# Kernel optimization log

Hardware: AMD Instinct MI355X
Metric: run time of the kernel (lower is better)

The kernel has to match this reference:

```python
import jax, jax.numpy as jnp
from jax import lax
import numpy as np

NEG_SLOPE = 0.01  # torch leaky_relu default
KSIZE = 5

def lrelu(x):
    return jax.nn.leaky_relu(x, NEG_SLOPE)

def conv(x, w, b):
    # x: [N,C,H,W], w: [O,I,kh,kw], valid padding (pad=False in ConvChain)
    y = lax.conv_general_dilated(x, w, (1, 1), 'VALID',
                                 dimension_numbers=('NCHW', 'OIHW', 'NCHW'))
    return y + b[None, :, None, None]

def _forward(features, radiance, global_features,
             emb_w0, emb_b0, emb_w, emb_b,
             pf_w0, pf_b0, pf_w1, pf_b1, pf_w2, pf_b2,
             sf_w, sf_b,
             kp_w0, kp_b0, kp_w1, kp_b1, kp_w2, kp_b2):
    bs, spp, nf, h, w = features.shape
    ngf = global_features.shape[1]
    K = KSIZE

    # --- sample_embedding over all samples at once (replaces per-sp loop) ---
    g = jnp.broadcast_to(global_features, (bs, ngf, h, w))
    x = jnp.concatenate(
        [jnp.broadcast_to(g[:, None], (bs, spp, ngf, h, w)), features], axis=2)
    x = x.reshape(bs * spp, ngf + nf, h, w)
    x = lrelu(conv(x, emb_w0, emb_b0))
    for i in range(5):  # hidden conv layers 1..5
        x = lrelu(conv(x, emb_w[i], emb_b[i]))
    x = conv(x, emb_w[5], emb_b[5])  # linear output layer
    pixel_embed = x.reshape(bs, spp, x.shape[1], x.shape[2], x.shape[3]).max(axis=1)

    # --- pixel_features chain (3 layers, last linear) ---
    p = lrelu(conv(pixel_embed, pf_w0, pf_b0))
    p = lrelu(conv(p, pf_w1, pf_b1))
    pfeat = conv(p, pf_w2, pf_b2)  # [bs, pair_width, ph, pw]
    ph, pw = pfeat.shape[2], pfeat.shape[3]

    # --- crop features/radiance so needed = ph + K - 1 ---
    needed = ph + K - 1
    crop = (h - needed) // 2
    feat_c = features[..., crop:crop + needed, crop:crop + needed]
    rad_c = radiance[..., crop:crop + needed, crop:crop + needed]

    # --- gather K*K taps per pixel (unfold) ---
    taps = jnp.stack([feat_c[..., dy:dy + ph, dx:dx + pw]
                      for dy in range(K) for dx in range(K)], axis=0)
    # [K,K,bs,spp,nf,ph,pw] -> [bs,ph,pw,spp,ky,kx,nf]
    taps = taps.reshape(K, K, bs, spp, nf, ph, pw).transpose(2, 5, 6, 3, 0, 1, 4)
    off = jnp.arange(K, dtype=taps.dtype) - K // 2
    taps = taps.at[..., 0].add(off)            # x += kx - K//2 (kx axis)
    taps = taps.at[..., 1].add(off[:, None])   # y += ky - K//2 (ky axis)

    rt = jnp.stack([rad_c[..., dy:dy + ph, dx:dx + pw]
                    for dy in range(K) for dx in range(K)], axis=0)
    # [K,K,bs,spp,3,ph,pw] -> [bs,3,ph,pw,spp,ky,kx]
    rt = rt.reshape(K, K, bs, spp, 3, ph, pw).transpose(2, 4, 5, 6, 3, 0, 1)

    # --- sample_features: single linear layer (FullyConnected depth=1) ---
    sf = jnp.einsum('...f,of->...o', taps, sf_w) + sf_b  # [b,ph,pw,spp,ky,kx,pair]

    # --- kernel_predictor on pixel_features + sample_features ---
    pairf = pfeat.transpose(0, 2, 3, 1)[:, :, :, None, None, None, :]
    hdd = lrelu(jnp.einsum('...i,oi->...o', pairf + sf, kp_w0) + kp_b0)
    hdd = lrelu(jnp.einsum('...i,oi->...o', hdd, kp_w1) + kp_b1)
    wts = (jnp.einsum('...i,oi->...o', hdd, kp_w2) + kp_b2)[..., 0]  # [b,ph,pw,spp,ky,kx]

    # --- weighted radiance accumulate + normalize ---
    unnorm = jnp.einsum('bhwsyx,bchwsyx->bchw', wts, rt)
    sumw = wts.sum(axis=(3, 4, 5))[:, None]  # [b,1,ph,pw]
    return unnorm / (sumw + 1e-8)


def setup_inputs() -> dict:
    key = jax.random.key(0)
    ks = jax.random.split(key, 24)
    BS, SPP, NF, NGF, H, W = 1, 4, 12, 4, 116, 116
    WIDTH, PAIR = 128, 64
    s = 0.05
    inp = {}
    inp['features'] = jax.random.normal(ks[0], (BS, SPP, NF, H, W), jnp.float32)
    inp['radiance'] = jax.random.uniform(ks[1], (BS, SPP, 3, H, W), jnp.float32)
    inp['global_features'] = jax.random.normal(ks[2], (BS, NGF, 1, 1), jnp.float32)
    # sample_embedding: 7 conv layers (first 16->128, rest 128->128, last linear)
    inp['emb_w0'] = jax.random.normal(ks[3], (WIDTH, NF + NGF, 3, 3)) * s
    inp['emb_b0'] = jax.random.normal(ks[4], (WIDTH,)) * s
    inp['emb_w'] = jax.random.normal(ks[5], (6, WIDTH, WIDTH, 3, 3)) * s
    inp['emb_b'] = jax.random.normal(ks[6], (6, WIDTH)) * s
    # pixel_features: 3 conv layers 128->128->128->64 (last linear)
    inp['pf_w0'] = jax.random.normal(ks[7], (WIDTH, WIDTH, 3, 3)) * s
    inp['pf_b0'] = jax.random.normal(ks[8], (WIDTH,)) * s
    inp['pf_w1'] = jax.random.normal(ks[9], (WIDTH, WIDTH, 3, 3)) * s
    inp['pf_b1'] = jax.random.normal(ks[10], (WIDTH,)) * s
    inp['pf_w2'] = jax.random.normal(ks[11], (PAIR, WIDTH, 3, 3)) * s
    inp['pf_b2'] = jax.random.normal(ks[12], (PAIR,)) * s
    # sample_features: FullyConnected(12 -> 64, depth=1) = single linear
    inp['sf_w'] = jax.random.normal(ks[13], (PAIR, NF)) * s
    inp['sf_b'] = jax.random.normal(ks[14], (PAIR,)) * s
    # kernel_predictor: FullyConnected(64 -> 1, depth=3)
    inp['kp_w0'] = jax.random.normal(ks[15], (PAIR, PAIR)) * s
    inp['kp_b0'] = jax.random.normal(ks[16], (PAIR,)) * s
    inp['kp_w1'] = jax.random.normal(ks[17], (PAIR, PAIR)) * s
    inp['kp_b1'] = jax.random.normal(ks[18], (PAIR,)) * s
    inp['kp_w2'] = jax.random.normal(ks[19], (1, PAIR)) * s
    inp['kp_b2'] = jax.random.normal(ks[20], (1,)) * s
    return inp


def reference(features, radiance, global_features,
              emb_w0, emb_b0, emb_w, emb_b,
              pf_w0, pf_b0, pf_w1, pf_b1, pf_w2, pf_b2,
              sf_w, sf_b,
              kp_w0, kp_b0, kp_w1, kp_b1, kp_w2, kp_b2):
    return _forward(features, radiance, global_features,
                    emb_w0, emb_b0, emb_w, emb_b,
                    pf_w0, pf_b0, pf_w1, pf_b1, pf_w2, pf_b2,
                    sf_w, sf_b,
                    kp_w0, kp_b0, kp_w1, kp_b1, kp_w2, kp_b2)
```

## Files before the change

### kernel.cpp

```cpp
#include <hip/hip_runtime.h>


#define HW2 13456
#define NF  12
#define NGF 4

__device__ __forceinline__ float lrelu_f(float x) { return x > 0.f ? x : 0.01f * x; }

__global__ __launch_bounds__(256) void k_buildx0(const float* __restrict__ features,
                                                 const float* __restrict__ gf,
                                                 float* __restrict__ out) {
    int i = blockIdx.x * 256 + threadIdx.x;
    const int total = 4 * 16 * HW2;
    if (i >= total) return;
    int n  = i / (16 * HW2);
    int r  = i - n * (16 * HW2);
    int c  = r / HW2;
    int yx = r - c * HW2;
    float v = (c < NGF) ? gf[c] : features[(n * NF + (c - NGF)) * HW2 + yx];
    out[i] = v;
}

__global__ __launch_bounds__(256) void k_wt(const float* __restrict__ w,
                                            float* __restrict__ wt,
                                            int Cout, int Cin) {
    int i = blockIdx.x * 256 + threadIdx.x;
    int total = Cout * Cin * 9;
    if (i >= total) return;
    int m   = i / (Cin * 9);
    int r   = i - m * (Cin * 9);
    int cin = r / 9;
    int kyx = r - cin * 9;
    wt[(kyx * Cin + cin) * Cout + m] = w[i];
}

__global__ __launch_bounds__(256) void k_wt2(const float* __restrict__ w,
                                             float* __restrict__ wt) {
    int i = blockIdx.x * 256 + threadIdx.x;
    if (i >= 4096) return;
    int o = i >> 6, k = i & 63;
    wt[k * 64 + o] = w[i];
}

template <int CIN, int COUT>
__global__ __launch_bounds__(256) void k_convd(const float* __restrict__ in,
                                               const float* __restrict__ wt,
                                               const float* __restrict__ bias,
                                               float* __restrict__ out,
                                               int H, int W, int relu, int tout) {
    constexpr int MW = COUT / 4;
    const int OH = H - 2, OW = W - 2;
    const int n   = blockIdx.z;
    const int ty0 = blockIdx.y * 8, tx0 = blockIdx.x * 8;

    __shared__ float It[CIN * 100];

    const int tid = threadIdx.x;

    const float* inb = in + (size_t)n * CIN * H * W;
    for (int i = tid; i < CIN * 100; i += 256) {
        int cin = i / 100;
        int r   = i - cin * 100;
        int y   = r / 10;
        int x   = r - y * 10;
        int gy = ty0 + y; if (gy > H - 1) gy = H - 1;
        int gx = tx0 + x; if (gx > W - 1) gx = W - 1;
        It[i] = inb[((size_t)cin * H + gy) * W + gx];
    }
    __syncthreads();

    const int lane  = tid & 63;
    const int wv    = __builtin_amdgcn_readfirstlane(tid >> 6);
    const int ly    = lane >> 3, lx = lane & 7;
    const int lbase = ly * 10 + lx;

    float acc[MW];
    #pragma unroll
    for (int mi = 0; mi < MW; ++mi) acc[mi] = 0.f;

    for (int ky = 0; ky < 3; ++ky) {
        for (int kx = 0; kx < 3; ++kx) {
            const int kyx  = ky * 3 + kx;
            const int aoff = lbase + ky * 10 + kx;
            const float* wrow = wt + (size_t)kyx * CIN * COUT + wv * MW;
            #pragma unroll 8
            for (int cin = 0; cin < CIN; ++cin) {
                float v = It[cin * 100 + aoff];
                const float* wr = wrow + (size_t)cin * COUT;
                #pragma unroll
                for (int mi = 0; mi < MW; ++mi)
                    acc[mi] += wr[mi] * v;
            }
        }
    }

    int oy = ty0 + ly, ox = tx0 + lx;
    if (oy < OH && ox < OW) {
        if (tout) {
            float* ob = out + (size_t)(oy * OW + ox) * COUT;
            #pragma unroll
            for (int mi = 0; mi < MW; ++mi) {
                int m = wv * MW + mi;
                float val = acc[mi] + bias[m];
                if (relu) val = lrelu_f(val);
                ob[m] = val;
            }
        } else {
            #pragma unroll
            for (int mi = 0; mi < MW; ++mi) {
                int m = wv * MW + mi;
                float val = acc[mi] + bias[m];
                if (relu) val = lrelu_f(val);
                out[(((size_t)n * COUT + m) * OH + oy) * OW + ox] = val;
            }
        }
    }
}

__global__ __launch_bounds__(256) void k_sppmax(const float* __restrict__ in,
                                                float* __restrict__ out) {
    int i = blockIdx.x * 256 + threadIdx.x;
    const int total = 128 * 102 * 102;
    if (i >= total) return;
    float m = in[i];
    #pragma unroll
    for (int s = 1; s < 4; ++s) m = fmaxf(m, in[i + s * total]);
    out[i] = m;
}

__global__ __launch_bounds__(256) void k_mlp(const float* __restrict__ features,
                                             const float* __restrict__ pfeat_t,
                                             const float* __restrict__ sf_w,
                                             const float* __restrict__ sf_b,
                                             const float* __restrict__ w0t,
                                             const float* __restrict__ b0,
                                             const float* __restrict__ w1t,
                                             const float* __restrict__ b1,
                                             const float* __restrict__ w2, const float* __restrict__ b2,
                                             float* __restrict__ wts) {
    __shared__ float vx[64][256];
    const int t   = threadIdx.x;
    const int gid = blockIdx.x * 256 + t;
    {
        int p  = gid / 100;
        int r  = gid - p * 100;
        int s  = r / 25;
        int tp = r - s * 25;
        int dy = tp / 5;
        int dx = tp - dy * 5;
        int h  = p / 96;
        int w  = p - h * 96;

        int y = 8 + h + dy, x = 8 + w + dx;
        const float* fb = features + (size_t)(s * NF) * HW2 + (size_t)y * 116 + x;
        float f[12];
        #pragma unroll
        for (int i = 0; i < 12; ++i) f[i] = fb[i * HW2];
        f[0] += (float)(dx - 2);
        f[1] += (float)(dy - 2);

        const float* pft = pfeat_t + (size_t)p * 64;
        #pragma unroll
        for (int o = 0; o < 64; ++o) {
            float a = 0.f;
            #pragma unroll
            for (int i = 0; i < 12; ++i) a += sf_w[o * 12 + i] * f[i];
            a += sf_b[o];
            vx[o][t] = pft[o] + a;
        }
    }
    __syncthreads();

    const int lane = t & 63;
    const int og   = 16 * __builtin_amdgcn_readfirstlane(t >> 6);
    const int tl   = lane * 4;

    {
        float acc[16][4];
        #pragma unroll
        for (int j = 0; j < 16; ++j)
            #pragma unroll
            for (int c = 0; c < 4; ++c) acc[j][c] = 0.f;
        #pragma unroll 4
        for (int k = 0; k < 64; ++k) {
            float4 xv = *(const float4*)(&vx[k][tl]);
            const float* wr = w0t + k * 64 + og;
            #pragma unroll
            for (int j = 0; j < 16; ++j) {
                float wj = wr[j];
                acc[j][0] += wj * xv.x; acc[j][1] += wj * xv.y;
                acc[j][2] += wj * xv.z; acc[j][3] += wj * xv.w;
            }
        }
        __syncthreads();
        #pragma unroll
        for (int j = 0; j < 16; ++j) {
            float bj = b0[og + j];
            float4 ov;
            ov.x = lrelu_f(acc[j][0] + bj); ov.y = lrelu_f(acc[j][1] + bj);
            ov.z = lrelu_f(acc[j][2] + bj); ov.w = lrelu_f(acc[j][3] + bj);
            *(float4*)(&vx[og + j][tl]) = ov;
        }
        __syncthreads();
    }

    {
        float acc[16][4];
        #pragma unroll
        for (int j = 0; j < 16; ++j)
            #pragma unroll
            for (int c = 0; c < 4; ++c) acc[j][c] = 0.f;
        #pragma unroll 4
        for (int k = 0; k < 64; ++k) {
            float4 xv = *(const float4*)(&vx[k][tl]);
            const float* wr = w1t + k * 64 + og;
            #pragma unroll
            for (int j = 0; j < 16; ++j) {
                float wj = wr[j];
                acc[j][0] += wj * xv.x; acc[j][1] += wj * xv.y;
                acc[j][2] += wj * xv.z; acc[j][3] += wj * xv.w;
            }
        }
        __syncthreads();
        #pragma unroll
        for (int j = 0; j < 16; ++j) {
            float bj = b1[og + j];
            float4 ov;
            ov.x = lrelu_f(acc[j][0] + bj); ov.y = lrelu_f(acc[j][1] + bj);
            ov.z = lrelu_f(acc[j][2] + bj); ov.w = lrelu_f(acc[j][3] + bj);
            *(float4*)(&vx[og + j][tl]) = ov;
        }
        __syncthreads();
    }

    {
        float a = 0.f;
        #pragma unroll
        for (int i = 0; i < 64; ++i) a += w2[i] * vx[i][t];
        a += b2[0];
        wts[gid] = a;
    }
}

__global__ __launch_bounds__(256) void k_reduce(const float* __restrict__ wts,
                                                const float* __restrict__ radiance,
                                                float* __restrict__ out) {
    int p = blockIdx.x * 256 + threadIdx.x;
    if (p >= 9216) return;
    int h = p / 96, w = p - h * 96;
    float sw = 0.f, un0 = 0.f, un1 = 0.f, un2 = 0.f;
    const float* wp = wts + (size_t)p * 100;
    for (int s = 0; s < 4; ++s) {
        #pragma unroll
        for (int dy = 0; dy < 5; ++dy) {
            #pragma unroll
            for (int dx = 0; dx < 5; ++dx) {
                float wv = wp[s * 25 + dy * 5 + dx];
                sw += wv;
                int y = 8 + h + dy, x = 8 + w + dx;
                const float* rb = radiance + (size_t)(s * 3) * HW2 + (size_t)y * 116 + x;
                un0 += wv * rb[0 * HW2];
                un1 += wv * rb[1 * HW2];
                un2 += wv * rb[2 * HW2];
            }
        }
    }
    float inv = 1.f / (sw + 1e-8f);
    out[0 * 9216 + p] = un0 * inv;
    out[1 * 9216 + p] = un1 * inv;
    out[2 * 9216 + p] = un2 * inv;
}

extern "C" void kernel_launch(void* const* d_in, const int* in_sizes, int n_in,
                              void* d_out, int out_size, void* d_ws, size_t ws_size,
                              hipStream_t stream) {
    const float* features = (const float*)d_in[0];
    const float* radiance = (const float*)d_in[1];
    const float* gf       = (const float*)d_in[2];
    const float* emb_w0   = (const float*)d_in[3];
    const float* emb_b0   = (const float*)d_in[4];
    const float* emb_w    = (const float*)d_in[5];
    const float* emb_b    = (const float*)d_in[6];
    const float* pf_w0    = (const float*)d_in[7];
    const float* pf_b0    = (const float*)d_in[8];
    const float* pf_w1    = (const float*)d_in[9];
    const float* pf_b1    = (const float*)d_in[10];
    const float* pf_w2    = (const float*)d_in[11];
    const float* pf_b2    = (const float*)d_in[12];
    const float* sf_w     = (const float*)d_in[13];
    const float* sf_b     = (const float*)d_in[14];
    const float* kp_w0    = (const float*)d_in[15];
    const float* kp_b0    = (const float*)d_in[16];
    const float* kp_w1    = (const float*)d_in[17];
    const float* kp_b1    = (const float*)d_in[18];
    const float* kp_w2    = (const float*)d_in[19];
    const float* kp_b2    = (const float*)d_in[20];
    float* out = (float*)d_out;

    float* WT = (float*)d_ws;
    float* wt0  = WT;
    float* wtE0 = WT + 18432;
    float* wtP0 = WT + 18432 + 6 * 147456;
    float* wtP1 = WT + 1050624;
    float* wtP2 = WT + 1198080;
    float* w0t  = WT + 1271808;
    float* w1t  = WT + 1275904;
    float* A = WT + 1280000;
    float* B = A + 6653952;

    auto wtr = [&](const float* w, float* dst, int Cout, int Cin) {
        int total = Cout * Cin * 9;
        k_wt<<<dim3((total + 255) / 256), 256, 0, stream>>>(w, dst, Cout, Cin);
    };
    wtr(emb_w0, wt0, 128, 16);
    for (int i = 0; i < 6; ++i) wtr(emb_w + i * 147456, wtE0 + i * 147456, 128, 128);
    wtr(pf_w0, wtP0, 128, 128);
    wtr(pf_w1, wtP1, 128, 128);
    wtr(pf_w2, wtP2, 64, 128);
    k_wt2<<<dim3(16), 256, 0, stream>>>(kp_w0, w0t);
    k_wt2<<<dim3(16), 256, 0, stream>>>(kp_w1, w1t);

    k_buildx0<<<dim3((4 * 16 * HW2 + 255) / 256), 256, 0, stream>>>(features, gf, A);

    auto grid8 = [](int OH, int OW, int N) {
        return dim3((OW + 7) / 8, (OH + 7) / 8, N);
    };

    k_convd<16, 128><<<grid8(114, 114, 4), 256, 0, stream>>>(A, wt0, emb_b0, B, 116, 116, 1, 0);
    k_convd<128,128><<<grid8(112, 112, 4), 256, 0, stream>>>(B, wtE0 + 0*147456, emb_b + 0*128, A, 114, 114, 1, 0);
    k_convd<128,128><<<grid8(110, 110, 4), 256, 0, stream>>>(A, wtE0 + 1*147456, emb_b + 1*128, B, 112, 112, 1, 0);
    k_convd<128,128><<<grid8(108, 108, 4), 256, 0, stream>>>(B, wtE0 + 2*147456, emb_b + 2*128, A, 110, 110, 1, 0);
    k_convd<128,128><<<grid8(106, 106, 4), 256, 0, stream>>>(A, wtE0 + 3*147456, emb_b + 3*128, B, 108, 108, 1, 0);
    k_convd<128,128><<<grid8(104, 104, 4), 256, 0, stream>>>(B, wtE0 + 4*147456, emb_b + 4*128, A, 106, 106, 1, 0);
    k_convd<128,128><<<grid8(102, 102, 4), 256, 0, stream>>>(A, wtE0 + 5*147456, emb_b + 5*128, B, 104, 104, 0, 0);

    k_sppmax<<<dim3(1331712 / 256), 256, 0, stream>>>(B, A);

    k_convd<128,128><<<grid8(100, 100, 1), 256, 0, stream>>>(A, wtP0, pf_b0, B, 102, 102, 1, 0);
    k_convd<128,128><<<grid8(98,  98,  1), 256, 0, stream>>>(B, wtP1, pf_b1, A, 100, 100, 1, 0);
    k_convd<128, 64><<<grid8(96,  96,  1), 256, 0, stream>>>(A, wtP2, pf_b2, B, 98,  98,  0, 1);

    k_mlp<<<dim3(3600), 256, 0, stream>>>(features, B, sf_w, sf_b,
                                          w0t, kp_b0, w1t, kp_b1, kp_w2, kp_b2, A);

    k_reduce<<<dim3(36), 256, 0, stream>>>(A, radiance, out);
}
```

Before: 2.643 ms.

## Replace LDS-tiled conv with direct-load kernel splitting output channels across blocks

The 3x3 conv kernel no longer stages an input tile in shared memory. Each thread now reads its input taps straight from global memory and computes two output rows across 16 output channels per wave, and output channels are split into 64-wide groups on the grid z axis. The launch-bounds occupancy hint is raised to 3 blocks. This removes the LDS fill and the barrier and cuts register pressure from 32 accumulators to 32 split across two pixels, giving more blocks. The cost is more global and cache traffic, since input values are re-read per kernel tap and per channel group with no explicit reuse.

```diff
diff --git a/kernel.cpp b/kernel.cpp
--- a/kernel.cpp
+++ b/kernel.cpp
@@ -42,76 +42,77 @@
     wt[k * 64 + o] = w[i];
 }
 
-template <int CIN, int COUT>
-__global__ __launch_bounds__(256) void k_convd(const float* __restrict__ in,
-                                               const float* __restrict__ wt,
-                                               const float* __restrict__ bias,
-                                               float* __restrict__ out,
-                                               int H, int W, int relu, int tout) {
-    constexpr int MW = COUT / 4;
+template <int CIN>
+__global__ __launch_bounds__(256, 3) void k_convg(const float* __restrict__ in,
+                                                  const float* __restrict__ wt,
+                                                  const float* __restrict__ bias,
+                                                  float* __restrict__ out,
+                                                  int H, int W, int COUT,
+                                                  int relu, int tout) {
     const int OH = H - 2, OW = W - 2;
-    const int n   = blockIdx.z;
-    const int ty0 = blockIdx.y * 8, tx0 = blockIdx.x * 8;
-
-    __shared__ float It[CIN * 100];
-
-    const int tid = threadIdx.x;
+    const int MB = COUT >> 6;
+    const int z  = blockIdx.z;
+    const int n  = z / MB;
+    const int mh = z - n * MB;
+
+    const int tid  = threadIdx.x, lane = tid & 63;
+    const int wv   = __builtin_amdgcn_readfirstlane(tid >> 6);
+    const int mbase = mh * 64 + wv * 16;
+    const int ly = lane >> 3, lx = lane & 7;
+    const int oy0 = blockIdx.y * 16 + ly;
+    const int oy1 = oy0 + 8;
+    const int ox  = blockIdx.x * 8 + lx;
+    const int cy0 = min(oy0, OH - 1), cy1 = min(oy1, OH - 1), cx = min(ox, OW - 1);
 
     const float* inb = in + (size_t)n * CIN * H * W;
-    for (int i = tid; i < CIN * 100; i += 256) {
-        int cin = i / 100;
-        int r   = i - cin * 100;
-        int y   = r / 10;
-        int x   = r - y * 10;
-        int gy = ty0 + y; if (gy > H - 1) gy = H - 1;
-        int gx = tx0 + x; if (gx > W - 1) gx = W - 1;
-        It[i] = inb[((size_t)cin * H + gy) * W + gx];
-    }
-    __syncthreads();
-
-    const int lane  = tid & 63;
-    const int wv    = __builtin_amdgcn_readfirstlane(tid >> 6);
-    const int ly    = lane >> 3, lx = lane & 7;
-    const int lbase = ly * 10 + lx;
-
-    float acc[MW];
+    const int HW = H * W;
+
+    float acc[16][2];
     #pragma unroll
-    for (int mi = 0; mi < MW; ++mi) acc[mi] = 0.f;
-
+    for (int mi = 0; mi < 16; ++mi) { acc[mi][0] = 0.f; acc[mi][1] = 0.f; }
+
+    #pragma unroll
     for (int ky = 0; ky < 3; ++ky) {
+        #pragma unroll
         for (int kx = 0; kx < 3; ++kx) {
-            const int kyx  = ky * 3 + kx;
-            const int aoff = lbase + ky * 10 + kx;
-            const float* wrow = wt + (size_t)kyx * CIN * COUT + wv * MW;
-            #pragma unroll 8
+            const float* ia = inb + (cy0 + ky) * W + (cx + kx);
+            const float* ib = inb + (cy1 + ky) * W + (cx + kx);
+            const float* wr = wt + (size_t)((ky * 3 + kx) * CIN) * COUT + mbase;
             for (int cin = 0; cin < CIN; ++cin) {
-                float v = It[cin * 100 + aoff];
-                const float* wr = wrow + (size_t)cin * COUT;
+                float v0 = ia[cin * HW];
+                float v1 = ib[cin * HW];
+                const float* w = wr + cin * COUT;
                 #pragma unroll
-                for (int mi = 0; mi < MW; ++mi)
-                    acc[mi] += wr[mi] * v;
-            }
-        }
-    }
-
-    int oy = ty0 + ly, ox = tx0 + lx;
-    if (oy < OH && ox < OW) {
-        if (tout) {
-            float* ob = out + (size_t)(oy * OW + ox) * COUT;
-            #pragma unroll
-            for (int mi = 0; mi < MW; ++mi) {
-                int m = wv * MW + mi;
-                float val = acc[mi] + bias[m];
-                if (relu) val = lrelu_f(val);
-                ob[m] = val;
-            }
-        } else {
-            #pragma unroll
-            for (int mi = 0; mi < MW; ++mi) {
-                int m = wv * MW + mi;
-                float val = acc[mi] + bias[m];
-                if (relu) val = lrelu_f(val);
-                out[(((size_t)n * COUT + m) * OH + oy) * OW + ox] = val;
+                for (int mi = 0; mi < 16; ++mi) {
+                    acc[mi][0] += w[mi] * v0;
+                    acc[mi][1] += w[mi] * v1;
+                }
+            }
+        }
+    }
+
+    if (ox < OW) {
+        #pragma unroll
+        for (int p = 0; p < 2; ++p) {
+            int oy = p ? oy1 : oy0;
+            if (oy >= OH) continue;
+            if (tout) {
+                float* ob = out + (size_t)(oy * OW + ox) * COUT;
+                #pragma unroll
+                for (int mi = 0; mi < 16; ++mi) {
+                    int m = mbase + mi;
+                    float val = acc[mi][p] + bias[m];
+                    if (relu) val = lrelu_f(val);
+                    ob[m] = val;
+                }
+            } else {
+                #pragma unroll
+                for (int mi = 0; mi < 16; ++mi) {
+                    int m = mbase + mi;
+                    float val = acc[mi][p] + bias[m];
+                    if (relu) val = lrelu_f(val);
+                    out[(((size_t)n * COUT + m) * OH + oy) * OW + ox] = val;
+                }
             }
         }
     }
@@ -322,23 +323,24 @@
 
     k_buildx0<<<dim3((4 * 16 * HW2 + 255) / 256), 256, 0, stream>>>(features, gf, A);
 
-    auto grid8 = [](int OH, int OW, int N) {
-        return dim3((OW + 7) / 8, (OH + 7) / 8, N);
+    auto gridc = [](int H, int W, int N, int COUT) {
+        int OH = H - 2, OW = W - 2;
+        return dim3((OW + 7) / 8, (OH + 15) / 16, N * (COUT >> 6));
     };
 
-    k_convd<16, 128><<<grid8(114, 114, 4), 256, 0, stream>>>(A, wt0, emb_b0, B, 116, 116, 1, 0);
-    k_convd<128,128><<<grid8(112, 112, 4), 256, 0, stream>>>(B, wtE0 + 0*147456, emb_b + 0*128, A, 114, 114, 1, 0);
-    k_convd<128,128><<<grid8(110, 110, 4), 256, 0, stream>>>(A, wtE0 + 1*147456, emb_b + 1*128, B, 112, 112, 1, 0);
-    k_convd<128,128><<<grid8(108, 108, 4), 256, 0, stream>>>(B, wtE0 + 2*147456, emb_b + 2*128, A, 110, 110, 1, 0);
-    k_convd<128,128><<<grid8(106, 106, 4), 256, 0, stream>>>(A, wtE0 + 3*147456, emb_b + 3*128, B, 108, 108, 1, 0);
-    k_convd<128,128><<<grid8(104, 104, 4), 256, 0, stream>>>(B, wtE0 + 4*147456, emb_b + 4*128, A, 106, 106, 1, 0);
-    k_convd<128,128><<<grid8(102, 102, 4), 256, 0, stream>>>(A, wtE0 + 5*147456, emb_b + 5*128, B, 104, 104, 0, 0);
+    k_convg<16><<<gridc(116, 116, 4, 128), 256, 0, stream>>>(A, wt0, emb_b0, B, 116, 116, 128, 1, 0);
+    k_convg<128><<<gridc(114, 114, 4, 128), 256, 0, stream>>>(B, wtE0 + 0*147456, emb_b + 0*128, A, 114, 114, 128, 1, 0);
+    k_convg<128><<<gridc(112, 112, 4, 128), 256, 0, stream>>>(A, wtE0 + 1*147456, emb_b + 1*128, B, 112, 112, 128, 1, 0);
+    k_convg<128><<<gridc(110, 110, 4, 128), 256, 0, stream>>>(B, wtE0 + 2*147456, emb_b + 2*128, A, 110, 110, 128, 1, 0);
+    k_convg<128><<<gridc(108, 108, 4, 128), 256, 0, stream>>>(A, wtE0 + 3*147456, emb_b + 3*128, B, 108, 108, 128, 1, 0);
+    k_convg<128><<<gridc(106, 106, 4, 128), 256, 0, stream>>>(B, wtE0 + 4*147456, emb_b + 4*128, A, 106, 106, 128, 1, 0);
+    k_convg<128><<<gridc(104, 104, 4, 128), 256, 0, stream>>>(A, wtE0 + 5*147456, emb_b + 5*128, B, 104, 104, 128, 0, 0);
 
     k_sppmax<<<dim3(1331712 / 256), 256, 0, stream>>>(B, A);
 
-    k_convd<128,128><<<grid8(100, 100, 1), 256, 0, stream>>>(A, wtP0, pf_b0, B, 102, 102, 1, 0);
-    k_convd<128,128><<<grid8(98,  98,  1), 256, 0, stream>>>(B, wtP1, pf_b1, A, 100, 100, 1, 0);
-    k_convd<128, 64><<<grid8(96,  96,  1), 256, 0, stream>>>(A, wtP2, pf_b2, B, 98,  98,  0, 1);
+    k_convg<128><<<gridc(102, 102, 1, 128), 256, 0, stream>>>(A, wtP0, pf_b0, B, 102, 102, 128, 1, 0);
+    k_convg<128><<<gridc(100, 100, 1, 128), 256, 0, stream>>>(B, wtP1, pf_b1, A, 100, 100, 128, 1, 0);
+    k_convg<128><<<gridc(98,  98,  1, 64),  256, 0, stream>>>(A, wtP2, pf_b2, B, 98,  98,  64,  0, 1);
 
     k_mlp<<<dim3(3600), 256, 0, stream>>>(features, B, sf_w, sf_b,
                                           w0t, kp_b0, w1t, kp_b1, kp_w2, kp_b2, A);
```

Result: slower. 2.937 ms (+11.1%).

## Replace LDS-tiled direct conv with global-load conv using 8 wavefronts per block

Applied to the files above, without the earlier changes.

The 3x3 convolution kernel stops staging a 10x10 input halo tile in shared memory and has each lane read inputs directly from global memory, relying on the cache. Each block now covers 32x2 output pixels with 512 threads, and each of its 8 wavefronts computes 16 output channels instead of 32. The aim is to drop the shared-memory fill and barrier, raise occupancy and halve per-thread accumulator registers. The cost is more global and L1/L2 traffic for repeated input reads and more redundant scalar weight loads across wavefronts.

```diff
diff --git a/kernel.cpp b/kernel.cpp
--- a/kernel.cpp
+++ b/kernel.cpp
@@ -43,64 +43,52 @@
 }
 
 template <int CIN, int COUT>
-__global__ __launch_bounds__(256) void k_convd(const float* __restrict__ in,
+__global__ __launch_bounds__(512) void k_convw(const float* __restrict__ in,
                                                const float* __restrict__ wt,
                                                const float* __restrict__ bias,
                                                float* __restrict__ out,
                                                int H, int W, int relu, int tout) {
-    constexpr int MW = COUT / 4;
+    constexpr int MW = COUT / 8;
     const int OH = H - 2, OW = W - 2;
     const int n   = blockIdx.z;
-    const int ty0 = blockIdx.y * 8, tx0 = blockIdx.x * 8;
-
-    __shared__ float It[CIN * 100];
-
-    const int tid = threadIdx.x;
+    const int tid = threadIdx.x, lane = tid & 63;
+    const int wv  = __builtin_amdgcn_readfirstlane(tid >> 6);
+    const int mbase = wv * MW;
+    const int lx = lane & 31, lyh = lane >> 5;
+    const int oy = blockIdx.y * 2 + lyh;
+    const int ox = blockIdx.x * 32 + lx;
+    const int cx = min(ox, OW - 1);
 
     const float* inb = in + (size_t)n * CIN * H * W;
-    for (int i = tid; i < CIN * 100; i += 256) {
-        int cin = i / 100;
-        int r   = i - cin * 100;
-        int y   = r / 10;
-        int x   = r - y * 10;
-        int gy = ty0 + y; if (gy > H - 1) gy = H - 1;
-        int gx = tx0 + x; if (gx > W - 1) gx = W - 1;
-        It[i] = inb[((size_t)cin * H + gy) * W + gx];
-    }
-    __syncthreads();
-
-    const int lane  = tid & 63;
-    const int wv    = __builtin_amdgcn_readfirstlane(tid >> 6);
-    const int ly    = lane >> 3, lx = lane & 7;
-    const int lbase = ly * 10 + lx;
+    const int HW = H * W;
 
     float acc[MW];
     #pragma unroll
     for (int mi = 0; mi < MW; ++mi) acc[mi] = 0.f;
 
+    #pragma unroll
     for (int ky = 0; ky < 3; ++ky) {
+        #pragma unroll
         for (int kx = 0; kx < 3; ++kx) {
-            const int kyx  = ky * 3 + kx;
-            const int aoff = lbase + ky * 10 + kx;
-            const float* wrow = wt + (size_t)kyx * CIN * COUT + wv * MW;
-            #pragma unroll 8
+            const float* ia = inb + (oy + ky) * W + (cx + kx);
+            const float* wr = wt + (size_t)((ky * 3 + kx) * CIN) * COUT + mbase;
+            #pragma unroll 2
             for (int cin = 0; cin < CIN; ++cin) {
-                float v = It[cin * 100 + aoff];
-                const float* wr = wrow + (size_t)cin * COUT;
+                float v = ia[cin * HW];
+                const float* w = wr + cin * COUT;
                 #pragma unroll
                 for (int mi = 0; mi < MW; ++mi)
-                    acc[mi] += wr[mi] * v;
-            }
-        }
-    }
-
-    int oy = ty0 + ly, ox = tx0 + lx;
-    if (oy < OH && ox < OW) {
+                    acc[mi] += w[mi] * v;
+            }
+        }
+    }
+
+    if (ox < OW) {
         if (tout) {
             float* ob = out + (size_t)(oy * OW + ox) * COUT;
             #pragma unroll
             for (int mi = 0; mi < MW; ++mi) {
-                int m = wv * MW + mi;
+                int m = mbase + mi;
                 float val = acc[mi] + bias[m];
                 if (relu) val = lrelu_f(val);
                 ob[m] = val;
@@ -108,7 +96,7 @@
         } else {
             #pragma unroll
             for (int mi = 0; mi < MW; ++mi) {
-                int m = wv * MW + mi;
+                int m = mbase + mi;
                 float val = acc[mi] + bias[m];
                 if (relu) val = lrelu_f(val);
                 out[(((size_t)n * COUT + m) * OH + oy) * OW + ox] = val;
@@ -322,23 +310,24 @@
 
     k_buildx0<<<dim3((4 * 16 * HW2 + 255) / 256), 256, 0, stream>>>(features, gf, A);
 
-    auto grid8 = [](int OH, int OW, int N) {
-        return dim3((OW + 7) / 8, (OH + 7) / 8, N);
+    auto gridc = [](int H, int W, int N) {
+        int OH = H - 2, OW = W - 2;
+        return dim3((OW + 31) / 32, OH / 2, N);
     };
 
-    k_convd<16, 128><<<grid8(114, 114, 4), 256, 0, stream>>>(A, wt0, emb_b0, B, 116, 116, 1, 0);
-    k_convd<128,128><<<grid8(112, 112, 4), 256, 0, stream>>>(B, wtE0 + 0*147456, emb_b + 0*128, A, 114, 114, 1, 0);
-    k_convd<128,128><<<grid8(110, 110, 4), 256, 0, stream>>>(A, wtE0 + 1*147456, emb_b + 1*128, B, 112, 112, 1, 0);
-    k_convd<128,128><<<grid8(108, 108, 4), 256, 0, stream>>>(B, wtE0 + 2*147456, emb_b + 2*128, A, 110, 110, 1, 0);
-    k_convd<128,128><<<grid8(106, 106, 4), 256, 0, stream>>>(A, wtE0 + 3*147456, emb_b + 3*128, B, 108, 108, 1, 0);
-    k_convd<128,128><<<grid8(104, 104, 4), 256, 0, stream>>>(B, wtE0 + 4*147456, emb_b + 4*128, A, 106, 106, 1, 0);
-    k_convd<128,128><<<grid8(102, 102, 4), 256, 0, stream>>>(A, wtE0 + 5*147456, emb_b + 5*128, B, 104, 104, 0, 0);
+    k_convw<16, 128><<<gridc(116, 116, 4), 512, 0, stream>>>(A, wt0, emb_b0, B, 116, 116, 1, 0);
+    k_convw<128,128><<<gridc(114, 114, 4), 512, 0, stream>>>(B, wtE0 + 0*147456, emb_b + 0*128, A, 114, 114, 1, 0);
+    k_convw<128,128><<<gridc(112, 112, 4), 512, 0, stream>>>(A, wtE0 + 1*147456, emb_b + 1*128, B, 112, 112, 1, 0);
+    k_convw<128,128><<<gridc(110, 110, 4), 512, 0, stream>>>(B, wtE0 + 2*147456, emb_b + 2*128, A, 110, 110, 1, 0);
+    k_convw<128,128><<<gridc(108, 108, 4), 512, 0, stream>>>(A, wtE0 + 3*147456, emb_b + 3*128, B, 108, 108, 1, 0);
+    k_convw<128,128><<<gridc(106, 106, 4), 512, 0, stream>>>(B, wtE0 + 4*147456, emb_b + 4*128, A, 106, 106, 1, 0);
+    k_convw<128,128><<<gridc(104, 104, 4), 512, 0, stream>>>(A, wtE0 + 5*147456, emb_b + 5*128, B, 104, 104, 0, 0);
 
     k_sppmax<<<dim3(1331712 / 256), 256, 0, stream>>>(B, A);
 
-    k_convd<128,128><<<grid8(100, 100, 1), 256, 0, stream>>>(A, wtP0, pf_b0, B, 102, 102, 1, 0);
-    k_convd<128,128><<<grid8(98,  98,  1), 256, 0, stream>>>(B, wtP1, pf_b1, A, 100, 100, 1, 0);
-    k_convd<128, 64><<<grid8(96,  96,  1), 256, 0, stream>>>(A, wtP2, pf_b2, B, 98,  98,  0, 1);
+    k_convw<128,128><<<gridc(102, 102, 1), 512, 0, stream>>>(A, wtP0, pf_b0, B, 102, 102, 1, 0);
+    k_convw<128,128><<<gridc(100, 100, 1), 512, 0, stream>>>(B, wtP1, pf_b1, A, 100, 100, 1, 0);
+    k_convw<128, 64><<<gridc(98,  98,  1), 512, 0, stream>>>(A, wtP2, pf_b2, B, 98,  98,  0, 1);
 
     k_mlp<<<dim3(3600), 256, 0, stream>>>(features, B, sf_w, sf_b,
                                           w0t, kp_b0, w1t, kp_b1, kp_w2, kp_b2, A);
```

Result: faster. 2.329 ms (-11.9%).
